# Kernel optimization log

Measured on AMD Instinct MI355X. Metric: run time of the kernel, lower is better.

## Reference

```python
import jax, jax.numpy as jnp
import numpy as np

L, H = 2, 512  # num_layers, hidden_dim (== input_dim)

def setup_inputs() -> dict:
    key = jax.random.key(0)
    ks = jax.random.split(key, 9)
    T, B, D = 1024, 64, 512
    s = 0.05  # scale randn params to keep gates non-saturated
    return {
        "x":   jax.random.normal(ks[0], (T, B, D), jnp.float32),
        "Wii": jax.random.normal(ks[1], (L, 3 * H, D), jnp.float32) * s,
        "Wic": jax.random.normal(ks[2], (L, 3 * H, H), jnp.float32) * s,
        "Wih": jax.random.normal(ks[3], (L, 3 * H, H), jnp.float32) * s,
        "bii": jax.random.normal(ks[4], (L, 3 * H), jnp.float32) * s,
        "bic": jax.random.normal(ks[5], (L, 3 * H), jnp.float32) * s,
        "bih": jax.random.normal(ks[6], (L, 3 * H), jnp.float32) * s,
        "Whh": jax.random.normal(ks[7], (L, H, H), jnp.float32) * s,
        "bhh": jax.random.normal(ks[8], (L, H), jnp.float32) * s,
    }

def _res_lstm_layer(xs, Wii, Wic, Wih, bii, bic, bih, Whh, bhh):
    # xs: [T, B, D]; input_size == hidden_size so residual is identity add.
    T, B, _ = xs.shape
    bias = bii + bic + bih  # fold the three gate biases once
    def step(carry, x_t):
        hx, cx = carry
        gates = (jnp.matmul(x_t, Wii.T) + jnp.matmul(hx, Wih.T)
                 + jnp.matmul(cx, Wic.T) + bias)          # [B, 3H]
        i_g, f_g, o_g = jnp.split(gates, 3, axis=1)
        cellgate = jnp.tanh(jnp.matmul(hx, Whh.T) + bhh)    # [B, H]
        cy = jax.nn.sigmoid(f_g) * cx + jax.nn.sigmoid(i_g) * cellgate
        hy = jax.nn.sigmoid(o_g) * (jnp.tanh(cy) + x_t)     # residual
        return (hy, cy), hy
    init = (jnp.zeros((B, H), xs.dtype), jnp.zeros((B, H), xs.dtype))
    (h, c), outs = jax.lax.scan(step, init, xs)
    return outs, h, c

def reference(x, Wii, Wic, Wih, bii, bic, bih, Whh, bhh):
    outs = x
    h_list, c_list = [], []
    for l in range(L):  # small fixed layer count
        outs, h, c = _res_lstm_layer(outs, Wii[l], Wic[l], Wih[l],
                                     bii[l], bic[l], bih[l], Whh[l], bhh[l])
        h_list.append(h)
        c_list.append(c)
    h_n = jnp.stack(h_list, axis=0)  # [L, B, H]
    c_n = jnp.stack(c_list, axis=0)
    return outs, h_n, c_n
```

## Files before the change

kernel.cpp:

```cpp
#include <hip/hip_runtime.h>
#include <cstdint>

typedef unsigned short u16;
typedef unsigned int   u32;
typedef __bf16 v8bf  __attribute__((ext_vector_type(8)));
typedef float  v4f   __attribute__((ext_vector_type(4)));
typedef u32    u32x2 __attribute__((ext_vector_type(2)));
typedef u32    u32x4 __attribute__((ext_vector_type(4)));

#define T_STEPS 1024
#define G3 1536

#define OFF_RING0 0ull
#define OFF_RING1 1048576ull
#define OFF_XBF   0ull
#define OFF_XG    67108864ull
#define OFF_WII   268435456ull
#define OFF_WPACK 270008320ull
#define OFF_WPK2  277348352ull
#define OFF_BIASF 278921216ull

__device__ __forceinline__ u16 f2b(float f) {
  u32 u = __builtin_bit_cast(u32, f);
  u += 0x7fffu + ((u >> 16) & 1u);
  return (u16)(u >> 16);
}
__device__ __forceinline__ float b2f(u16 h) {
  u32 u = ((u32)h) << 16;
  return __builtin_bit_cast(float, u);
}
__device__ __forceinline__ float sigm(float x) { return 1.0f / (1.0f + __expf(-x)); }


__global__ void k_cvt(const float* __restrict__ s, u16* __restrict__ d, int n4) {
  int i = blockIdx.x * blockDim.x + threadIdx.x;
  int st = gridDim.x * blockDim.x;
  for (; i < n4; i += st) {
    float4 v = reinterpret_cast<const float4*>(s)[i];
    u32 lo = (u32)f2b(v.x) | ((u32)f2b(v.y) << 16);
    u32 hi = (u32)f2b(v.z) | ((u32)f2b(v.w) << 16);
    uint2 pk; pk.x = lo; pk.y = hi;
    reinterpret_cast<uint2*>(d)[i] = pk;
  }
}

__global__ void k_fold(const float* __restrict__ a, const float* __restrict__ b,
                       const float* __restrict__ c, float* __restrict__ o, int n) {
  int i = blockIdx.x * blockDim.x + threadIdx.x;
  if (i < n) o[i] = a[i] + b[i] + c[i];
}

__global__ void k_pack(const float* __restrict__ Wih, const float* __restrict__ Wic,
                       const float* __restrict__ Whh, u16* __restrict__ wp) {
  int t = blockIdx.x * blockDim.x + threadIdx.x;
  if (t >= 2 * 32 * 112 * 64) return;
  int lane = t & 63; int rest = t >> 6;
  int c = rest % 112; rest /= 112;
  int s = rest & 31; int l = rest >> 5;
  int col16 = lane & 15, kq = lane >> 4;
  const float* src;
  if (c < 96) {
    int tau = c >> 5, kk = c & 31;
    int col = tau * 512 + s * 16 + col16;
    int k = kk * 32 + kq * 8;
    src = (k < 512) ? (Wih + ((size_t)l * G3 + col) * 512 + k)
                    : (Wic + ((size_t)l * G3 + col) * 512 + (k - 512));
  } else {
    int kk = c - 96;
    int col = s * 16 + col16;
    int k = kk * 32 + kq * 8;
    src = Whh + ((size_t)l * 512 + col) * 512 + k;
  }
  u16 o[8];
#pragma unroll
  for (int i = 0; i < 8; ++i) o[i] = f2b(src[i]);
  uint4 v;
  v.x = (u32)o[0] | ((u32)o[1] << 16);
  v.y = (u32)o[2] | ((u32)o[3] << 16);
  v.z = (u32)o[4] | ((u32)o[5] << 16);
  v.w = (u32)o[6] | ((u32)o[7] << 16);
  reinterpret_cast<uint4*>(wp)[t] = v;
}

__global__ void k_pack2(const float* __restrict__ Wii, u16* __restrict__ wp2) {
  int t = blockIdx.x * blockDim.x + threadIdx.x;
  if (t >= 32 * 3 * 16 * 64) return;
  int lane = t & 63;
  int kk = (t >> 6) & 15;
  int w = (t >> 10) % 3;
  int s = t / 3072;
  int col = w * 512 + s * 16 + (lane & 15);
  int k = kk * 32 + (lane >> 4) * 8;
  const float* src = Wii + ((size_t)G3 + col) * 512 + k;
  u16 o[8];
#pragma unroll
  for (int i = 0; i < 8; ++i) o[i] = f2b(src[i]);
  uint4 v;
  v.x = (u32)o[0] | ((u32)o[1] << 16);
  v.y = (u32)o[2] | ((u32)o[3] << 16);
  v.z = (u32)o[4] | ((u32)o[5] << 16);
  v.w = (u32)o[6] | ((u32)o[7] << 16);
  reinterpret_cast<uint4*>(wp2)[t] = v;
}


__global__ __launch_bounds__(256) void k_gemm(const u16* __restrict__ A,
                                              const u16* __restrict__ Bt,
                                              u16* __restrict__ C) {
  __shared__ u16 As[128 * 40];
  __shared__ u16 Bs[128 * 40];
  int m0 = blockIdx.x * 128, n0 = blockIdx.y * 128;
  int tid = threadIdx.x, lane = tid & 63, w = tid >> 6, wr = w >> 1, wc = w & 1;
  int rl = lane & 15, kq = lane >> 4;
  v4f acc[4][4] = {};
  for (int k0 = 0; k0 < 512; k0 += 32) {
#pragma unroll
    for (int c = tid; c < 1024; c += 256) {
      int row = (c & 511) >> 2, q = c & 3;
      const u16* src = (c < 512) ? (A + (size_t)(m0 + row) * 512 + k0 + q * 8)
                                 : (Bt + (size_t)(n0 + row) * 512 + k0 + q * 8);
      uint4 v = *reinterpret_cast<const uint4*>(src);
      u16* dst = (c < 512) ? (As + row * 40 + q * 8) : (Bs + row * 40 + q * 8);
      *reinterpret_cast<uint4*>(dst) = v;
    }
    __syncthreads();
    v8bf a[4], b[4];
#pragma unroll
    for (int mi = 0; mi < 4; ++mi)
      a[mi] = *reinterpret_cast<const v8bf*>(As + (wr * 64 + mi * 16 + rl) * 40 + kq * 8);
#pragma unroll
    for (int ni = 0; ni < 4; ++ni)
      b[ni] = *reinterpret_cast<const v8bf*>(Bs + (wc * 64 + ni * 16 + rl) * 40 + kq * 8);
#pragma unroll
    for (int mi = 0; mi < 4; ++mi)
#pragma unroll
      for (int ni = 0; ni < 4; ++ni)
        acc[mi][ni] = __builtin_amdgcn_mfma_f32_16x16x32_bf16(a[mi], b[ni], acc[mi][ni], 0, 0, 0);
    __syncthreads();
  }
#pragma unroll
  for (int mi = 0; mi < 4; ++mi)
#pragma unroll
    for (int ni = 0; ni < 4; ++ni)
#pragma unroll
      for (int r = 0; r < 4; ++r) {
        int row = m0 + wr * 64 + mi * 16 + kq * 4 + r;
        int col = n0 + wc * 64 + ni * 16 + rl;
        C[(size_t)row * G3 + col] = f2b(acc[mi][ni][r]);
      }
}


__global__ __launch_bounds__(512, 1) void k_lstm(
    const u16* __restrict__ xg, const u16* __restrict__ wp, const u16* __restrict__ wp2,
    const float* __restrict__ biasf, const float* __restrict__ bhh,
    const float* __restrict__ xin, float* __restrict__ outs,
    float* __restrict__ hn, float* __restrict__ cn,
    char* __restrict__ ring0, char* __restrict__ ring1) {
  extern __shared__ char lds[];
  u16* alds   = (u16*)lds;
  float* olds = (float*)(lds + 65792);
  u16* w1lds  = (u16*)(lds + 73984);
  int tid = threadIdx.x, lane = tid & 63, w = tid >> 6;
  int w2 = w >> 1, half = w & 1;
  int blk = blockIdx.x, g = blk >> 5, s = blk & 31;

  int erow = (tid >> 4) & 15, ecol = tid & 15;
  int bglob = g * 16 + erow, hcol = s * 16 + ecol;
  int col16 = lane & 15, kq = lane >> 4;
  bool isGate = (w2 < 3);
  float bias0 = 0.0f, bias1 = 0.0f;
  int cbase, nch;
  if (isGate) {
    cbase = w2 * 32 + half * 16; nch = 16;
    if (half == 0) {
      bias0 = biasf[w2 * 512 + s * 16 + col16];
      bias1 = biasf[1536 + w2 * 512 + s * 16 + col16];
    }
  } else {
    cbase = 96 + half * 8; nch = 8;
    if (half == 0) {
      bias0 = bhh[s * 16 + col16];
      bias1 = bhh[512 + s * 16 + col16];
    }
  }
  int colglob = w2 * 512 + s * 16 + col16;

  const u16* w0src = wp + (size_t)s * 57344 + (size_t)cbase * 512 + lane * 8;
  const u16* w1src = wp + 1835008 + (size_t)s * 57344 + (size_t)cbase * 512 + lane * 8;
  v8bf breg0[16], breg1[16];
  if (isGate) {
#pragma unroll
    for (int kk = 0; kk < 16; ++kk) {
      breg0[kk] = *reinterpret_cast<const v8bf*>(w0src + kk * 512);
      breg1[kk] = *reinterpret_cast<const v8bf*>(w1src + kk * 512);
    }
  } else {
#pragma unroll
    for (int kk = 0; kk < 8; ++kk) {
      breg0[kk] = *reinterpret_cast<const v8bf*>(w0src + kk * 512);
      breg1[kk] = *reinterpret_cast<const v8bf*>(w1src + kk * 512);
    }
  }
  {
    const uint4* src = reinterpret_cast<const uint4*>(wp2) + (size_t)s * 3072;
    for (int i = tid; i < 3072; i += 512)
      reinterpret_cast<uint4*>(w1lds)[i] = src[i];
  }
  float c0 = 0.0f, c1 = 0.0f;
  __syncthreads();

  auto Af = [&](int base, int kg) {
    return *reinterpret_cast<const v8bf*>(alds + col16 * 2056 + base + kg * 32 + kq * 8);
  };

  for (int t = 0; t <= T_STEPS; ++t) {
    bool doL0 = (t < T_STEPS), doL1 = (t > 0);

    float seed0[4] = {0.f, 0.f, 0.f, 0.f};
    float xi0 = 0.0f;
    if (doL0) {
      if (isGate) {
        if (half == 0) {
          const u16* xgp = xg + (size_t)(t * 64 + g * 16 + kq * 4) * G3 + colglob;
#pragma unroll
          for (int r4 = 0; r4 < 4; ++r4) seed0[r4] = b2f(xgp[(size_t)r4 * G3]) + bias0;
        }
      } else if (half == 0) {
#pragma unroll
        for (int r4 = 0; r4 < 4; ++r4) seed0[r4] = bias0;
      }
      if (tid < 256) xi0 = xin[(size_t)(t * 64 + bglob) * 512 + hcol];
    }

    u32x4 r[8];
    {
      const char* pb = ring0 + ((size_t)(t & 3) * 4 + g) * 65536 + (size_t)tid * 16;
      u32 exp = (u32)t; bool ok = false; u32 it = 0;
      while (!ok) {
#pragma unroll
        for (int i = 0; i < 8; ++i)
          asm volatile("global_load_dwordx4 %0, %1, off sc0 sc1"
                       : "=v"(r[i]) : "v"(pb + (size_t)i * 8192) : "memory");
        asm volatile("s_waitcnt vmcnt(0)" ::: "memory");
        __builtin_amdgcn_sched_barrier(0);
        ok = true;
#pragma unroll
        for (int i = 0; i < 8; ++i) ok = ok && (r[i][1] == exp) && (r[i][3] == exp);
        if (!ok) { if (++it > (1u << 11)) break; __builtin_amdgcn_s_sleep(1); }
      }
      __builtin_amdgcn_sched_barrier(0);
#pragma unroll
      for (int i = 0; i < 8; ++i) {
        int p = tid + i * 512;
        int row = p >> 8, c2 = p & 255;
        u32 hw = (r[i][0] & 0xffffu) | (r[i][2] << 16);
        u32 cw = (r[i][0] >> 16) | (r[i][2] & 0xffff0000u);
        *reinterpret_cast<u32*>(alds + row * 2056 + 2 * c2) = hw;
        *reinterpret_cast<u32*>(alds + row * 2056 + 512 + 2 * c2) = cw;
      }
    }

    u32x4 r2[8];
    if (doL1) {
      const char* pb = ring1 + ((size_t)((t - 1) & 3) * 4 + g) * 65536 + (size_t)tid * 16;
#pragma unroll
      for (int i = 0; i < 8; ++i)
        asm volatile("global_load_dwordx4 %0, %1, off sc0 sc1"
                     : "=v"(r2[i]) : "v"(pb + (size_t)i * 8192) : "memory");
    }
    __syncthreads();

    if (doL0) {
      v4f ac0, ac1, ac2, ac3;
#pragma unroll
      for (int r4 = 0; r4 < 4; ++r4) { ac0[r4] = seed0[r4]; ac1[r4] = 0.f; ac2[r4] = 0.f; ac3[r4] = 0.f; }
      if (isGate) {
#pragma unroll
        for (int kk = 0; kk < 16; kk += 4) {
          int kg = half * 16 + kk;
          ac0 = __builtin_amdgcn_mfma_f32_16x16x32_bf16(Af(0, kg + 0), breg0[kk + 0], ac0, 0, 0, 0);
          ac1 = __builtin_amdgcn_mfma_f32_16x16x32_bf16(Af(0, kg + 1), breg0[kk + 1], ac1, 0, 0, 0);
          ac2 = __builtin_amdgcn_mfma_f32_16x16x32_bf16(Af(0, kg + 2), breg0[kk + 2], ac2, 0, 0, 0);
          ac3 = __builtin_amdgcn_mfma_f32_16x16x32_bf16(Af(0, kg + 3), breg0[kk + 3], ac3, 0, 0, 0);
        }
      } else {
#pragma unroll
        for (int kk = 0; kk < 8; kk += 4) {
          int kg = half * 8 + kk;
          ac0 = __builtin_amdgcn_mfma_f32_16x16x32_bf16(Af(0, kg + 0), breg0[kk + 0], ac0, 0, 0, 0);
          ac1 = __builtin_amdgcn_mfma_f32_16x16x32_bf16(Af(0, kg + 1), breg0[kk + 1], ac1, 0, 0, 0);
          ac2 = __builtin_amdgcn_mfma_f32_16x16x32_bf16(Af(0, kg + 2), breg0[kk + 2], ac2, 0, 0, 0);
          ac3 = __builtin_amdgcn_mfma_f32_16x16x32_bf16(Af(0, kg + 3), breg0[kk + 3], ac3, 0, 0, 0);
        }
      }
      v4f acc;
#pragma unroll
      for (int r4 = 0; r4 < 4; ++r4) acc[r4] = (ac0[r4] + ac1[r4]) + (ac2[r4] + ac3[r4]);
#pragma unroll
      for (int r4 = 0; r4 < 4; ++r4) olds[w * 256 + (kq * 4 + r4) * 16 + col16] = acc[r4];
      __syncthreads();

      if (tid < 256) {
        float gi = olds[tid] + olds[256 + tid];
        float gf = olds[512 + tid] + olds[768 + tid];
        float go = olds[1024 + tid] + olds[1280 + tid];
        float gg = olds[1536 + tid] + olds[1792 + tid];
        float i_s = sigm(gi), f_s = sigm(gf), o_s = sigm(go);
        float cg = tanhf(gg);
        float cy = f_s * c0 + i_s * cg;
        float hy = o_s * (tanhf(cy) + xi0);
        c0 = cy;
        u16 hyb = f2b(hy), cyb = f2b(cy);
        u32x2 pkt;
        pkt[0] = (u32)hyb | ((u32)cyb << 16);
        pkt[1] = (u32)(t + 1);
        void* pd = ring0 + ((size_t)((t + 1) & 3) * 4 + g) * 65536
                   + (size_t)(erow * 512 + hcol) * 8;
        asm volatile("global_store_dwordx2 %0, %1, off sc0 sc1"
                     :: "v"(pd), "v"(pkt) : "memory");
        if (t == T_STEPS - 1) {
          hn[bglob * 512 + hcol] = hy;
          cn[bglob * 512 + hcol] = cy;
        }
      }
    }

    if (doL1) {
      float xi1 = (tid < 256) ? b2f(alds[erow * 2056 + hcol]) : 0.0f;

      {
        const char* pb = ring1 + ((size_t)((t - 1) & 3) * 4 + g) * 65536 + (size_t)tid * 16;
        u32 exp = (u32)(t - 1); u32 it = 0;
        for (;;) {
          asm volatile("s_waitcnt vmcnt(0)" ::: "memory");
          __builtin_amdgcn_sched_barrier(0);
          bool ok = true;
#pragma unroll
          for (int i = 0; i < 8; ++i) ok = ok && (r2[i][1] == exp) && (r2[i][3] == exp);
          if (ok) break;
          if (++it > (1u << 11)) break;
          __builtin_amdgcn_s_sleep(1);
#pragma unroll
          for (int i = 0; i < 8; ++i)
            asm volatile("global_load_dwordx4 %0, %1, off sc0 sc1"
                         : "=v"(r2[i]) : "v"(pb + (size_t)i * 8192) : "memory");
        }
        __builtin_amdgcn_sched_barrier(0);
#pragma unroll
        for (int i = 0; i < 8; ++i) {
          int p = tid + i * 512;
          int row = p >> 8, c2 = p & 255;
          u32 hw = (r2[i][0] & 0xffffu) | (r2[i][2] << 16);
          u32 cw = (r2[i][0] >> 16) | (r2[i][2] & 0xffff0000u);
          *reinterpret_cast<u32*>(alds + row * 2056 + 1024 + 2 * c2) = hw;
          *reinterpret_cast<u32*>(alds + row * 2056 + 1536 + 2 * c2) = cw;
        }
      }
      __syncthreads();

      v4f ac0, ac1, ac2, ac3;
#pragma unroll
      for (int r4 = 0; r4 < 4; ++r4) { ac0[r4] = bias1; ac1[r4] = 0.f; ac2[r4] = 0.f; ac3[r4] = 0.f; }
      if (isGate) {
#pragma unroll
        for (int kk = 0; kk < 16; kk += 4) {
          int kg = half * 16 + kk;
          ac0 = __builtin_amdgcn_mfma_f32_16x16x32_bf16(Af(1024, kg + 0), breg1[kk + 0], ac0, 0, 0, 0);
          ac1 = __builtin_amdgcn_mfma_f32_16x16x32_bf16(Af(1024, kg + 1), breg1[kk + 1], ac1, 0, 0, 0);
          ac2 = __builtin_amdgcn_mfma_f32_16x16x32_bf16(Af(1024, kg + 2), breg1[kk + 2], ac2, 0, 0, 0);
          ac3 = __builtin_amdgcn_mfma_f32_16x16x32_bf16(Af(1024, kg + 3), breg1[kk + 3], ac3, 0, 0, 0);
        }
#pragma unroll
        for (int kx = 0; kx < 8; kx += 4) {
          int kg = half * 8 + kx;
          ac0 = __builtin_amdgcn_mfma_f32_16x16x32_bf16(Af(0, kg + 0),
                  *reinterpret_cast<const v8bf*>(w1lds + ((w2 * 16 + kg + 0) * 64 + lane) * 8), ac0, 0, 0, 0);
          ac1 = __builtin_amdgcn_mfma_f32_16x16x32_bf16(Af(0, kg + 1),
                  *reinterpret_cast<const v8bf*>(w1lds + ((w2 * 16 + kg + 1) * 64 + lane) * 8), ac1, 0, 0, 0);
          ac2 = __builtin_amdgcn_mfma_f32_16x16x32_bf16(Af(0, kg + 2),
                  *reinterpret_cast<const v8bf*>(w1lds + ((w2 * 16 + kg + 2) * 64 + lane) * 8), ac2, 0, 0, 0);
          ac3 = __builtin_amdgcn_mfma_f32_16x16x32_bf16(Af(0, kg + 3),
                  *reinterpret_cast<const v8bf*>(w1lds + ((w2 * 16 + kg + 3) * 64 + lane) * 8), ac3, 0, 0, 0);
        }
      } else {
#pragma unroll
        for (int kk = 0; kk < 8; kk += 4) {
          int kg = half * 8 + kk;
          ac0 = __builtin_amdgcn_mfma_f32_16x16x32_bf16(Af(1024, kg + 0), breg1[kk + 0], ac0, 0, 0, 0);
          ac1 = __builtin_amdgcn_mfma_f32_16x16x32_bf16(Af(1024, kg + 1), breg1[kk + 1], ac1, 0, 0, 0);
          ac2 = __builtin_amdgcn_mfma_f32_16x16x32_bf16(Af(1024, kg + 2), breg1[kk + 2], ac2, 0, 0, 0);
          ac3 = __builtin_amdgcn_mfma_f32_16x16x32_bf16(Af(1024, kg + 3), breg1[kk + 3], ac3, 0, 0, 0);
        }
      }
      v4f acc;
#pragma unroll
      for (int r4 = 0; r4 < 4; ++r4) acc[r4] = (ac0[r4] + ac1[r4]) + (ac2[r4] + ac3[r4]);
#pragma unroll
      for (int r4 = 0; r4 < 4; ++r4) olds[w * 256 + (kq * 4 + r4) * 16 + col16] = acc[r4];
      __syncthreads();

      if (tid < 256) {
        float gi = olds[tid] + olds[256 + tid];
        float gf = olds[512 + tid] + olds[768 + tid];
        float go = olds[1024 + tid] + olds[1280 + tid];
        float gg = olds[1536 + tid] + olds[1792 + tid];
        float i_s = sigm(gi), f_s = sigm(gf), o_s = sigm(go);
        float cg = tanhf(gg);
        float cy = f_s * c1 + i_s * cg;
        float hy = o_s * (tanhf(cy) + xi1);
        c1 = cy;
        u16 hyb = f2b(hy), cyb = f2b(cy);
        u32x2 pkt;
        pkt[0] = (u32)hyb | ((u32)cyb << 16);
        pkt[1] = (u32)t;
        void* pd = ring1 + ((size_t)(t & 3) * 4 + g) * 65536
                   + (size_t)(erow * 512 + hcol) * 8;
        asm volatile("global_store_dwordx2 %0, %1, off sc0 sc1"
                     :: "v"(pd), "v"(pkt) : "memory");
        outs[(size_t)((t - 1) * 64 + bglob) * 512 + hcol] = hy;
        if (t == T_STEPS) {
          hn[32768 + bglob * 512 + hcol] = hy;
          cn[32768 + bglob * 512 + hcol] = cy;
        }
      }
    }
    __syncthreads();
  }
}


extern "C" void kernel_launch(void* const* d_in, const int* in_sizes, int n_in,
                              void* d_out, int out_size, void* d_ws, size_t ws_size,
                              hipStream_t stream) {
  const float* x   = (const float*)d_in[0];
  const float* Wii = (const float*)d_in[1];
  const float* Wic = (const float*)d_in[2];
  const float* Wih = (const float*)d_in[3];
  const float* bii = (const float*)d_in[4];
  const float* bic = (const float*)d_in[5];
  const float* bih = (const float*)d_in[6];
  const float* Whh = (const float*)d_in[7];
  const float* bhh = (const float*)d_in[8];
  float* out = (float*)d_out;
  char* ws = (char*)d_ws;

  u16* xbf     = (u16*)(ws + OFF_XBF);
  u16* xgb     = (u16*)(ws + OFF_XG);
  u16* wiib    = (u16*)(ws + OFF_WII);
  u16* wpack   = (u16*)(ws + OFF_WPACK);
  u16* wpk2    = (u16*)(ws + OFF_WPK2);
  float* biasf = (float*)(ws + OFF_BIASF);

  hipFuncSetAttribute(reinterpret_cast<const void*>(k_lstm),
                      hipFuncAttributeMaxDynamicSharedMemorySize, 123136);

  k_cvt <<<2048, 256, 0, stream>>>(x, xbf, 8388608);
  k_cvt <<<768, 256, 0, stream>>>(Wii, wiib, 196608);
  k_fold<<<12, 256, 0, stream>>>(bii, bic, bih, biasf, 3072);
  k_pack<<<1792, 256, 0, stream>>>(Wih, Wic, Whh, wpack);
  k_pack2<<<384, 256, 0, stream>>>(Wii, wpk2);
  k_gemm<<<dim3(512, 12), 256, 0, stream>>>(xbf, wiib, xgb);

  hipMemsetAsync(ws + OFF_RING0, 0, 2097152, stream);

  float* hn = out + 33554432;
  float* cn = out + 33554432 + 65536;
  k_lstm<<<128, 512, 123136, stream>>>(
      xgb, wpack, wpk2, biasf, bhh, x, out, hn, cn,
      ws + OFF_RING0, ws + OFF_RING1);
}
```

Measured before the change: 5.538 ms.

## Split layer-0 and layer-1 across wave groups with LDS counter sync

Waves 0-3 now handle layer 0 and waves 4-7 handle layer 1, so both layers' matvecs run concurrently instead of one after the other. Each wave holds a full K range of weights in registers, which removes the split-K partial-sum reduction. The two ring polls are merged into one loop that retries only the slices not yet ready. The per-layer __syncthreads is replaced by LDS atomic counters with spin-waits, at the cost of twice the register weights per wave and the risk of busy-wait contention.

```diff
diff --git a/kernel.cpp b/kernel.cpp
--- a/kernel.cpp
+++ b/kernel.cpp
@@ -161,53 +161,41 @@
   u16* alds   = (u16*)lds;
   float* olds = (float*)(lds + 65792);
   u16* w1lds  = (u16*)(lds + 73984);
+  u32* scnt   = (u32*)(lds + 123136);
   int tid = threadIdx.x, lane = tid & 63, w = tid >> 6;
-  int w2 = w >> 1, half = w & 1;
+  bool isL1 = w >= 4;
+  int wg = w & 3;
   int blk = blockIdx.x, g = blk >> 5, s = blk & 31;
 
-  int erow = (tid >> 4) & 15, ecol = tid & 15;
+  int et = tid & 255;
+  int erow = et >> 4, ecol = et & 15;
   int bglob = g * 16 + erow, hcol = s * 16 + ecol;
   int col16 = lane & 15, kq = lane >> 4;
-  bool isGate = (w2 < 3);
-  float bias0 = 0.0f, bias1 = 0.0f;
-  int cbase, nch;
+  bool isGate = (wg < 3);
+  float bias_w;
+  int cbase, nfr;
   if (isGate) {
-    cbase = w2 * 32 + half * 16; nch = 16;
-    if (half == 0) {
-      bias0 = biasf[w2 * 512 + s * 16 + col16];
-      bias1 = biasf[1536 + w2 * 512 + s * 16 + col16];
-    }
+    cbase = wg * 32; nfr = 32;
+    bias_w = biasf[(isL1 ? 1536 : 0) + wg * 512 + s * 16 + col16];
   } else {
-    cbase = 96 + half * 8; nch = 8;
-    if (half == 0) {
-      bias0 = bhh[s * 16 + col16];
-      bias1 = bhh[512 + s * 16 + col16];
-    }
-  }
-  int colglob = w2 * 512 + s * 16 + col16;
-
-  const u16* w0src = wp + (size_t)s * 57344 + (size_t)cbase * 512 + lane * 8;
-  const u16* w1src = wp + 1835008 + (size_t)s * 57344 + (size_t)cbase * 512 + lane * 8;
-  v8bf breg0[16], breg1[16];
-  if (isGate) {
-#pragma unroll
-    for (int kk = 0; kk < 16; ++kk) {
-      breg0[kk] = *reinterpret_cast<const v8bf*>(w0src + kk * 512);
-      breg1[kk] = *reinterpret_cast<const v8bf*>(w1src + kk * 512);
-    }
-  } else {
-#pragma unroll
-    for (int kk = 0; kk < 8; ++kk) {
-      breg0[kk] = *reinterpret_cast<const v8bf*>(w0src + kk * 512);
-      breg1[kk] = *reinterpret_cast<const v8bf*>(w1src + kk * 512);
-    }
-  }
+    cbase = 96; nfr = 16;
+    bias_w = bhh[(isL1 ? 512 : 0) + s * 16 + col16];
+  }
+  int colglob = wg * 512 + s * 16 + col16;
+
+  const u16* wsrc = wp + (isL1 ? 1835008u : 0u) + (size_t)s * 57344
+                    + (size_t)cbase * 512 + lane * 8;
+  v8bf breg[32];
+#pragma unroll
+  for (int kk = 0; kk < 32; ++kk)
+    if (kk < nfr) breg[kk] = *reinterpret_cast<const v8bf*>(wsrc + kk * 512);
   {
     const uint4* src = reinterpret_cast<const uint4*>(wp2) + (size_t)s * 3072;
     for (int i = tid; i < 3072; i += 512)
       reinterpret_cast<uint4*>(w1lds)[i] = src[i];
   }
-  float c0 = 0.0f, c1 = 0.0f;
+  if (tid < 2) scnt[tid] = 0;
+  float c_st = 0.0f;
   __syncthreads();
 
   auto Af = [&](int base, int kg) {
@@ -217,100 +205,114 @@
   for (int t = 0; t <= T_STEPS; ++t) {
     bool doL0 = (t < T_STEPS), doL1 = (t > 0);
 
-    float seed0[4] = {0.f, 0.f, 0.f, 0.f};
+    float seed[4] = {0.f, 0.f, 0.f, 0.f};
     float xi0 = 0.0f;
-    if (doL0) {
+    if (!isL1 && doL0) {
       if (isGate) {
-        if (half == 0) {
-          const u16* xgp = xg + (size_t)(t * 64 + g * 16 + kq * 4) * G3 + colglob;
-#pragma unroll
-          for (int r4 = 0; r4 < 4; ++r4) seed0[r4] = b2f(xgp[(size_t)r4 * G3]) + bias0;
-        }
-      } else if (half == 0) {
-#pragma unroll
-        for (int r4 = 0; r4 < 4; ++r4) seed0[r4] = bias0;
+        const u16* xgp = xg + (size_t)(t * 64 + g * 16 + kq * 4) * G3 + colglob;
+#pragma unroll
+        for (int r4 = 0; r4 < 4; ++r4) seed[r4] = b2f(xgp[(size_t)r4 * G3]) + bias_w;
+      } else {
+#pragma unroll
+        for (int r4 = 0; r4 < 4; ++r4) seed[r4] = bias_w;
       }
       if (tid < 256) xi0 = xin[(size_t)(t * 64 + bglob) * 512 + hcol];
     }
 
-    u32x4 r[8];
+    u32x4 r0[8], r1[8];
     {
-      const char* pb = ring0 + ((size_t)(t & 3) * 4 + g) * 65536 + (size_t)tid * 16;
-      u32 exp = (u32)t; bool ok = false; u32 it = 0;
-      while (!ok) {
-#pragma unroll
-        for (int i = 0; i < 8; ++i)
+      const char* pb0 = ring0 + ((size_t)(t & 3) * 4 + g) * 65536 + (size_t)tid * 16;
+      const char* pb1 = ring1 + ((size_t)((t - 1) & 3) * 4 + g) * 65536 + (size_t)tid * 16;
+      u32 exp0 = (u32)t, exp1 = (u32)(t - 1);
+      u32 m0 = 0xffu, m1 = doL1 ? 0xffu : 0u;
+      u32 it = 0;
+      for (;;) {
+#pragma unroll
+        for (int i = 0; i < 8; ++i) if ((m0 >> i) & 1)
           asm volatile("global_load_dwordx4 %0, %1, off sc0 sc1"
-                       : "=v"(r[i]) : "v"(pb + (size_t)i * 8192) : "memory");
+                       : "=v"(r0[i]) : "v"(pb0 + (size_t)i * 8192) : "memory");
+#pragma unroll
+        for (int i = 0; i < 8; ++i) if ((m1 >> i) & 1)
+          asm volatile("global_load_dwordx4 %0, %1, off sc0 sc1"
+                       : "=v"(r1[i]) : "v"(pb1 + (size_t)i * 8192) : "memory");
         asm volatile("s_waitcnt vmcnt(0)" ::: "memory");
         __builtin_amdgcn_sched_barrier(0);
-        ok = true;
-#pragma unroll
-        for (int i = 0; i < 8; ++i) ok = ok && (r[i][1] == exp) && (r[i][3] == exp);
-        if (!ok) { if (++it > (1u << 11)) break; __builtin_amdgcn_s_sleep(1); }
+#pragma unroll
+        for (int i = 0; i < 8; ++i)
+          if ((r0[i][1] == exp0) && (r0[i][3] == exp0)) m0 &= ~(1u << i);
+#pragma unroll
+        for (int i = 0; i < 8; ++i)
+          if ((r1[i][1] == exp1) && (r1[i][3] == exp1)) m1 &= ~(1u << i);
+        if (!(m0 | m1)) break;
+        if (++it > (1u << 11)) break;
+        __builtin_amdgcn_s_sleep(1);
       }
       __builtin_amdgcn_sched_barrier(0);
 #pragma unroll
       for (int i = 0; i < 8; ++i) {
         int p = tid + i * 512;
         int row = p >> 8, c2 = p & 255;
-        u32 hw = (r[i][0] & 0xffffu) | (r[i][2] << 16);
-        u32 cw = (r[i][0] >> 16) | (r[i][2] & 0xffff0000u);
+        u32 hw = (r0[i][0] & 0xffffu) | (r0[i][2] << 16);
+        u32 cw = (r0[i][0] >> 16) | (r0[i][2] & 0xffff0000u);
         *reinterpret_cast<u32*>(alds + row * 2056 + 2 * c2) = hw;
         *reinterpret_cast<u32*>(alds + row * 2056 + 512 + 2 * c2) = cw;
       }
-    }
-
-    u32x4 r2[8];
-    if (doL1) {
-      const char* pb = ring1 + ((size_t)((t - 1) & 3) * 4 + g) * 65536 + (size_t)tid * 16;
-#pragma unroll
-      for (int i = 0; i < 8; ++i)
-        asm volatile("global_load_dwordx4 %0, %1, off sc0 sc1"
-                     : "=v"(r2[i]) : "v"(pb + (size_t)i * 8192) : "memory");
+      if (doL1) {
+#pragma unroll
+        for (int i = 0; i < 8; ++i) {
+          int p = tid + i * 512;
+          int row = p >> 8, c2 = p & 255;
+          u32 hw = (r1[i][0] & 0xffffu) | (r1[i][2] << 16);
+          u32 cw = (r1[i][0] >> 16) | (r1[i][2] & 0xffff0000u);
+          *reinterpret_cast<u32*>(alds + row * 2056 + 1024 + 2 * c2) = hw;
+          *reinterpret_cast<u32*>(alds + row * 2056 + 1536 + 2 * c2) = cw;
+        }
+      }
     }
     __syncthreads();
 
-    if (doL0) {
-      v4f ac0, ac1, ac2, ac3;
-#pragma unroll
-      for (int r4 = 0; r4 < 4; ++r4) { ac0[r4] = seed0[r4]; ac1[r4] = 0.f; ac2[r4] = 0.f; ac3[r4] = 0.f; }
-      if (isGate) {
-#pragma unroll
-        for (int kk = 0; kk < 16; kk += 4) {
-          int kg = half * 16 + kk;
-          ac0 = __builtin_amdgcn_mfma_f32_16x16x32_bf16(Af(0, kg + 0), breg0[kk + 0], ac0, 0, 0, 0);
-          ac1 = __builtin_amdgcn_mfma_f32_16x16x32_bf16(Af(0, kg + 1), breg0[kk + 1], ac1, 0, 0, 0);
-          ac2 = __builtin_amdgcn_mfma_f32_16x16x32_bf16(Af(0, kg + 2), breg0[kk + 2], ac2, 0, 0, 0);
-          ac3 = __builtin_amdgcn_mfma_f32_16x16x32_bf16(Af(0, kg + 3), breg0[kk + 3], ac3, 0, 0, 0);
-        }
-      } else {
-#pragma unroll
-        for (int kk = 0; kk < 8; kk += 4) {
-          int kg = half * 8 + kk;
-          ac0 = __builtin_amdgcn_mfma_f32_16x16x32_bf16(Af(0, kg + 0), breg0[kk + 0], ac0, 0, 0, 0);
-          ac1 = __builtin_amdgcn_mfma_f32_16x16x32_bf16(Af(0, kg + 1), breg0[kk + 1], ac1, 0, 0, 0);
-          ac2 = __builtin_amdgcn_mfma_f32_16x16x32_bf16(Af(0, kg + 2), breg0[kk + 2], ac2, 0, 0, 0);
-          ac3 = __builtin_amdgcn_mfma_f32_16x16x32_bf16(Af(0, kg + 3), breg0[kk + 3], ac3, 0, 0, 0);
-        }
-      }
-      v4f acc;
-#pragma unroll
-      for (int r4 = 0; r4 < 4; ++r4) acc[r4] = (ac0[r4] + ac1[r4]) + (ac2[r4] + ac3[r4]);
-#pragma unroll
-      for (int r4 = 0; r4 < 4; ++r4) olds[w * 256 + (kq * 4 + r4) * 16 + col16] = acc[r4];
-      __syncthreads();
-
-      if (tid < 256) {
-        float gi = olds[tid] + olds[256 + tid];
-        float gf = olds[512 + tid] + olds[768 + tid];
-        float go = olds[1024 + tid] + olds[1280 + tid];
-        float gg = olds[1536 + tid] + olds[1792 + tid];
+    if (!isL1) {
+      if (doL0) {
+        v4f ac0, ac1, ac2, ac3;
+#pragma unroll
+        for (int r4 = 0; r4 < 4; ++r4) { ac0[r4] = seed[r4]; ac1[r4] = 0.f; ac2[r4] = 0.f; ac3[r4] = 0.f; }
+        if (isGate) {
+#pragma unroll
+          for (int kk = 0; kk < 32; kk += 4) {
+            ac0 = __builtin_amdgcn_mfma_f32_16x16x32_bf16(Af(0, kk + 0), breg[kk + 0], ac0, 0, 0, 0);
+            ac1 = __builtin_amdgcn_mfma_f32_16x16x32_bf16(Af(0, kk + 1), breg[kk + 1], ac1, 0, 0, 0);
+            ac2 = __builtin_amdgcn_mfma_f32_16x16x32_bf16(Af(0, kk + 2), breg[kk + 2], ac2, 0, 0, 0);
+            ac3 = __builtin_amdgcn_mfma_f32_16x16x32_bf16(Af(0, kk + 3), breg[kk + 3], ac3, 0, 0, 0);
+          }
+        } else {
+#pragma unroll
+          for (int kk = 0; kk < 16; kk += 4) {
+            ac0 = __builtin_amdgcn_mfma_f32_16x16x32_bf16(Af(0, kk + 0), breg[kk + 0], ac0, 0, 0, 0);
+            ac1 = __builtin_amdgcn_mfma_f32_16x16x32_bf16(Af(0, kk + 1), breg[kk + 1], ac1, 0, 0, 0);
+            ac2 = __builtin_amdgcn_mfma_f32_16x16x32_bf16(Af(0, kk + 2), breg[kk + 2], ac2, 0, 0, 0);
+            ac3 = __builtin_amdgcn_mfma_f32_16x16x32_bf16(Af(0, kk + 3), breg[kk + 3], ac3, 0, 0, 0);
+          }
+        }
+        v4f acc;
+#pragma unroll
+        for (int r4 = 0; r4 < 4; ++r4) acc[r4] = (ac0[r4] + ac1[r4]) + (ac2[r4] + ac3[r4]);
+#pragma unroll
+        for (int r4 = 0; r4 < 4; ++r4) olds[wg * 256 + (kq * 4 + r4) * 16 + col16] = acc[r4];
+        asm volatile("s_waitcnt lgkmcnt(0)" ::: "memory");
+        if (lane == 0) atomicAdd(&scnt[0], 1u);
+        {
+          volatile u32* vc = &scnt[0];
+          u32 tgt = 4u * (u32)(t + 1);
+          while (*vc < tgt) {}
+        }
+        __builtin_amdgcn_sched_barrier(0);
+
+        float gi = olds[et], gf = olds[256 + et], go = olds[512 + et], gg = olds[768 + et];
         float i_s = sigm(gi), f_s = sigm(gf), o_s = sigm(go);
         float cg = tanhf(gg);
-        float cy = f_s * c0 + i_s * cg;
+        float cy = f_s * c_st + i_s * cg;
         float hy = o_s * (tanhf(cy) + xi0);
-        c0 = cy;
+        c_st = cy;
         u16 hyb = f2b(hy), cyb = f2b(cy);
         u32x2 pkt;
         pkt[0] = (u32)hyb | ((u32)cyb << 16);
@@ -324,92 +326,60 @@
           cn[bglob * 512 + hcol] = cy;
         }
       }
-    }
-
-    if (doL1) {
-      float xi1 = (tid < 256) ? b2f(alds[erow * 2056 + hcol]) : 0.0f;
-
-      {
-        const char* pb = ring1 + ((size_t)((t - 1) & 3) * 4 + g) * 65536 + (size_t)tid * 16;
-        u32 exp = (u32)(t - 1); u32 it = 0;
-        for (;;) {
-          asm volatile("s_waitcnt vmcnt(0)" ::: "memory");
-          __builtin_amdgcn_sched_barrier(0);
-          bool ok = true;
-#pragma unroll
-          for (int i = 0; i < 8; ++i) ok = ok && (r2[i][1] == exp) && (r2[i][3] == exp);
-          if (ok) break;
-          if (++it > (1u << 11)) break;
-          __builtin_amdgcn_s_sleep(1);
-#pragma unroll
-          for (int i = 0; i < 8; ++i)
-            asm volatile("global_load_dwordx4 %0, %1, off sc0 sc1"
-                         : "=v"(r2[i]) : "v"(pb + (size_t)i * 8192) : "memory");
+    } else {
+      if (doL1) {
+        float xi1 = b2f(alds[erow * 2056 + hcol]);
+        v4f ac0, ac1, ac2, ac3;
+#pragma unroll
+        for (int r4 = 0; r4 < 4; ++r4) { ac0[r4] = bias_w; ac1[r4] = 0.f; ac2[r4] = 0.f; ac3[r4] = 0.f; }
+        if (isGate) {
+#pragma unroll
+          for (int kk = 0; kk < 32; kk += 4) {
+            ac0 = __builtin_amdgcn_mfma_f32_16x16x32_bf16(Af(1024, kk + 0), breg[kk + 0], ac0, 0, 0, 0);
+            ac1 = __builtin_amdgcn_mfma_f32_16x16x32_bf16(Af(1024, kk + 1), breg[kk + 1], ac1, 0, 0, 0);
+            ac2 = __builtin_amdgcn_mfma_f32_16x16x32_bf16(Af(1024, kk + 2), breg[kk + 2], ac2, 0, 0, 0);
+            ac3 = __builtin_amdgcn_mfma_f32_16x16x32_bf16(Af(1024, kk + 3), breg[kk + 3], ac3, 0, 0, 0);
+          }
+#pragma unroll
+          for (int kx = 0; kx < 16; kx += 4) {
+            ac0 = __builtin_amdgcn_mfma_f32_16x16x32_bf16(Af(0, kx + 0),
+                    *reinterpret_cast<const v8bf*>(w1lds + ((wg * 16 + kx + 0) * 64 + lane) * 8), ac0, 0, 0, 0);
+            ac1 = __builtin_amdgcn_mfma_f32_16x16x32_bf16(Af(0, kx + 1),
+                    *reinterpret_cast<const v8bf*>(w1lds + ((wg * 16 + kx + 1) * 64 + lane) * 8), ac1, 0, 0, 0);
+            ac2 = __builtin_amdgcn_mfma_f32_16x16x32_bf16(Af(0, kx + 2),
+                    *reinterpret_cast<const v8bf*>(w1lds + ((wg * 16 + kx + 2) * 64 + lane) * 8), ac2, 0, 0, 0);
+            ac3 = __builtin_amdgcn_mfma_f32_16x16x32_bf16(Af(0, kx + 3),
+                    *reinterpret_cast<const v8bf*>(w1lds + ((wg * 16 + kx + 3) * 64 + lane) * 8), ac3, 0, 0, 0);
+          }
+        } else {
+#pragma unroll
+          for (int kk = 0; kk < 16; kk += 4) {
+            ac0 = __builtin_amdgcn_mfma_f32_16x16x32_bf16(Af(1024, kk + 0), breg[kk + 0], ac0, 0, 0, 0);
+            ac1 = __builtin_amdgcn_mfma_f32_16x16x32_bf16(Af(1024, kk + 1), breg[kk + 1], ac1, 0, 0, 0);
+            ac2 = __builtin_amdgcn_mfma_f32_16x16x32_bf16(Af(1024, kk + 2), breg[kk + 2], ac2, 0, 0, 0);
+            ac3 = __builtin_amdgcn_mfma_f32_16x16x32_bf16(Af(1024, kk + 3), breg[kk + 3], ac3, 0, 0, 0);
+          }
+        }
+        v4f acc;
+#pragma unroll
+        for (int r4 = 0; r4 < 4; ++r4) acc[r4] = (ac0[r4] + ac1[r4]) + (ac2[r4] + ac3[r4]);
+#pragma unroll
+        for (int r4 = 0; r4 < 4; ++r4) olds[1024 + wg * 256 + (kq * 4 + r4) * 16 + col16] = acc[r4];
+        asm volatile("s_waitcnt lgkmcnt(0)" ::: "memory");
+        if (lane == 0) atomicAdd(&scnt[1], 1u);
+        {
+          volatile u32* vc = &scnt[1];
+          u32 tgt = 4u * (u32)t;
+          while (*vc < tgt) {}
         }
         __builtin_amdgcn_sched_barrier(0);
-#pragma unroll
-        for (int i = 0; i < 8; ++i) {
-          int p = tid + i * 512;
-          int row = p >> 8, c2 = p & 255;
-          u32 hw = (r2[i][0] & 0xffffu) | (r2[i][2] << 16);
-          u32 cw = (r2[i][0] >> 16) | (r2[i][2] & 0xffff0000u);
-          *reinterpret_cast<u32*>(alds + row * 2056 + 1024 + 2 * c2) = hw;
-          *reinterpret_cast<u32*>(alds + row * 2056 + 1536 + 2 * c2) = cw;
-        }
-      }
-      __syncthreads();
-
-      v4f ac0, ac1, ac2, ac3;
-#pragma unroll
-      for (int r4 = 0; r4 < 4; ++r4) { ac0[r4] = bias1; ac1[r4] = 0.f; ac2[r4] = 0.f; ac3[r4] = 0.f; }
-      if (isGate) {
-#pragma unroll
-        for (int kk = 0; kk < 16; kk += 4) {
-          int kg = half * 16 + kk;
-          ac0 = __builtin_amdgcn_mfma_f32_16x16x32_bf16(Af(1024, kg + 0), breg1[kk + 0], ac0, 0, 0, 0);
-          ac1 = __builtin_amdgcn_mfma_f32_16x16x32_bf16(Af(1024, kg + 1), breg1[kk + 1], ac1, 0, 0, 0);
-          ac2 = __builtin_amdgcn_mfma_f32_16x16x32_bf16(Af(1024, kg + 2), breg1[kk + 2], ac2, 0, 0, 0);
-          ac3 = __builtin_amdgcn_mfma_f32_16x16x32_bf16(Af(1024, kg + 3), breg1[kk + 3], ac3, 0, 0, 0);
-        }
-#pragma unroll
-        for (int kx = 0; kx < 8; kx += 4) {
-          int kg = half * 8 + kx;
-          ac0 = __builtin_amdgcn_mfma_f32_16x16x32_bf16(Af(0, kg + 0),
-                  *reinterpret_cast<const v8bf*>(w1lds + ((w2 * 16 + kg + 0) * 64 + lane) * 8), ac0, 0, 0, 0);
-          ac1 = __builtin_amdgcn_mfma_f32_16x16x32_bf16(Af(0, kg + 1),
-                  *reinterpret_cast<const v8bf*>(w1lds + ((w2 * 16 + kg + 1) * 64 + lane) * 8), ac1, 0, 0, 0);
-          ac2 = __builtin_amdgcn_mfma_f32_16x16x32_bf16(Af(0, kg + 2),
-                  *reinterpret_cast<const v8bf*>(w1lds + ((w2 * 16 + kg + 2) * 64 + lane) * 8), ac2, 0, 0, 0);
-          ac3 = __builtin_amdgcn_mfma_f32_16x16x32_bf16(Af(0, kg + 3),
-                  *reinterpret_cast<const v8bf*>(w1lds + ((w2 * 16 + kg + 3) * 64 + lane) * 8), ac3, 0, 0, 0);
-        }
-      } else {
-#pragma unroll
-        for (int kk = 0; kk < 8; kk += 4) {
-          int kg = half * 8 + kk;
-          ac0 = __builtin_amdgcn_mfma_f32_16x16x32_bf16(Af(1024, kg + 0), breg1[kk + 0], ac0, 0, 0, 0);
-          ac1 = __builtin_amdgcn_mfma_f32_16x16x32_bf16(Af(1024, kg + 1), breg1[kk + 1], ac1, 0, 0, 0);
-          ac2 = __builtin_amdgcn_mfma_f32_16x16x32_bf16(Af(1024, kg + 2), breg1[kk + 2], ac2, 0, 0, 0);
-          ac3 = __builtin_amdgcn_mfma_f32_16x16x32_bf16(Af(1024, kg + 3), breg1[kk + 3], ac3, 0, 0, 0);
-        }
-      }
-      v4f acc;
-#pragma unroll
-      for (int r4 = 0; r4 < 4; ++r4) acc[r4] = (ac0[r4] + ac1[r4]) + (ac2[r4] + ac3[r4]);
-#pragma unroll
-      for (int r4 = 0; r4 < 4; ++r4) olds[w * 256 + (kq * 4 + r4) * 16 + col16] = acc[r4];
-      __syncthreads();
-
-      if (tid < 256) {
-        float gi = olds[tid] + olds[256 + tid];
-        float gf = olds[512 + tid] + olds[768 + tid];
-        float go = olds[1024 + tid] + olds[1280 + tid];
-        float gg = olds[1536 + tid] + olds[1792 + tid];
+
+        float gi = olds[1024 + et], gf = olds[1280 + et], go = olds[1536 + et], gg = olds[1792 + et];
         float i_s = sigm(gi), f_s = sigm(gf), o_s = sigm(go);
         float cg = tanhf(gg);
-        float cy = f_s * c1 + i_s * cg;
+        float cy = f_s * c_st + i_s * cg;
         float hy = o_s * (tanhf(cy) + xi1);
-        c1 = cy;
+        c_st = cy;
         u16 hyb = f2b(hy), cyb = f2b(cy);
         u32x2 pkt;
         pkt[0] = (u32)hyb | ((u32)cyb << 16);
@@ -453,7 +423,7 @@
   float* biasf = (float*)(ws + OFF_BIASF);
 
   hipFuncSetAttribute(reinterpret_cast<const void*>(k_lstm),
-                      hipFuncAttributeMaxDynamicSharedMemorySize, 123136);
+                      hipFuncAttributeMaxDynamicSharedMemorySize, 123152);
 
   k_cvt <<<2048, 256, 0, stream>>>(x, xbf, 8388608);
   k_cvt <<<768, 256, 0, stream>>>(Wii, wiib, 196608);
@@ -466,7 +436,7 @@
 
   float* hn = out + 33554432;
   float* cn = out + 33554432 + 65536;
-  k_lstm<<<128, 512, 123136, stream>>>(
+  k_lstm<<<128, 512, 123152, stream>>>(
       xgb, wpack, wpk2, biasf, bhh, x, out, hn, cn,
       ws + OFF_RING0, ws + OFF_RING1);
 }
```

Result: slower. 5.944 ms, median of 2 (+7.3%).

## Replace per-element tagged ring packets with per-wave flag counters and merged phases

Applied to the files above, without the earlier changes.

Cross-block exchange of h/c state switches from 8-byte tagged packets, where every element carries the step number and is polled, to plain bf16 data in the ring plus a small array of per-wave flag words that consumers poll before one bulk load. This halves ring traffic and shrinks the poll to two dwords per lane. The layer-0 and layer-1 gate epilogues are also restructured so both layers' MFMA results go to separate LDS regions and share barriers, which removes some __syncthreads per step. In exchange, producers must wait for their data stores to complete before publishing the flag, adding a store-then-flag latency on the critical path.

```diff
diff --git a/kernel.cpp b/kernel.cpp
--- a/kernel.cpp
+++ b/kernel.cpp
@@ -5,20 +5,21 @@
 typedef unsigned int   u32;
 typedef __bf16 v8bf  __attribute__((ext_vector_type(8)));
 typedef float  v4f   __attribute__((ext_vector_type(4)));
-typedef u32    u32x2 __attribute__((ext_vector_type(2)));
 typedef u32    u32x4 __attribute__((ext_vector_type(4)));
 
 #define T_STEPS 1024
 #define G3 1536
 
-#define OFF_RING0 0ull
-#define OFF_RING1 1048576ull
-#define OFF_XBF   0ull
-#define OFF_XG    67108864ull
-#define OFF_WII   268435456ull
-#define OFF_WPACK 270008320ull
-#define OFF_WPK2  277348352ull
-#define OFF_BIASF 278921216ull
+#define OFF_RING0  0ull
+#define OFF_RING1  524288ull
+#define OFF_FLAGS0 1048576ull
+#define OFF_FLAGS1 1050624ull
+#define OFF_XBF    0ull
+#define OFF_XG     67108864ull
+#define OFF_WII    268435456ull
+#define OFF_WPACK  270008320ull
+#define OFF_WPK2   277348352ull
+#define OFF_BIASF  278921216ull
 
 __device__ __forceinline__ u16 f2b(float f) {
   u32 u = __builtin_bit_cast(u32, f);
@@ -156,11 +157,12 @@
     const float* __restrict__ biasf, const float* __restrict__ bhh,
     const float* __restrict__ xin, float* __restrict__ outs,
     float* __restrict__ hn, float* __restrict__ cn,
-    char* __restrict__ ring0, char* __restrict__ ring1) {
+    char* __restrict__ ring0, char* __restrict__ ring1,
+    u32* __restrict__ flags0, u32* __restrict__ flags1) {
   extern __shared__ char lds[];
   u16* alds   = (u16*)lds;
   float* olds = (float*)(lds + 65792);
-  u16* w1lds  = (u16*)(lds + 73984);
+  u16* w1lds  = (u16*)(lds + 82176);
   int tid = threadIdx.x, lane = tid & 63, w = tid >> 6;
   int w2 = w >> 1, half = w & 1;
   int blk = blockIdx.x, g = blk >> 5, s = blk & 31;
@@ -170,15 +172,15 @@
   int col16 = lane & 15, kq = lane >> 4;
   bool isGate = (w2 < 3);
   float bias0 = 0.0f, bias1 = 0.0f;
-  int cbase, nch;
+  int cbase;
   if (isGate) {
-    cbase = w2 * 32 + half * 16; nch = 16;
+    cbase = w2 * 32 + half * 16;
     if (half == 0) {
       bias0 = biasf[w2 * 512 + s * 16 + col16];
       bias1 = biasf[1536 + w2 * 512 + s * 16 + col16];
     }
   } else {
-    cbase = 96 + half * 8; nch = 8;
+    cbase = 96 + half * 8;
     if (half == 0) {
       bias0 = bhh[s * 16 + col16];
       bias1 = bhh[512 + s * 16 + col16];
@@ -210,6 +212,10 @@
   float c0 = 0.0f, c1 = 0.0f;
   __syncthreads();
 
+  const u32* fb0 = flags0 + g * 128;
+  const u32* fb1 = flags1 + g * 128;
+  int prow = tid >> 5, pcb = (tid & 31) * 32;
+
   auto Af = [&](int base, int kg) {
     return *reinterpret_cast<const v8bf*>(alds + col16 * 2056 + base + kg * 32 + kq * 8);
   };
@@ -220,54 +226,46 @@
     float seed0[4] = {0.f, 0.f, 0.f, 0.f};
     float xi0 = 0.0f;
     if (doL0) {
-      if (isGate) {
-        if (half == 0) {
+      if (half == 0) {
+        if (isGate) {
           const u16* xgp = xg + (size_t)(t * 64 + g * 16 + kq * 4) * G3 + colglob;
 #pragma unroll
           for (int r4 = 0; r4 < 4; ++r4) seed0[r4] = b2f(xgp[(size_t)r4 * G3]) + bias0;
-        }
-      } else if (half == 0) {
-#pragma unroll
-        for (int r4 = 0; r4 < 4; ++r4) seed0[r4] = bias0;
+        } else {
+#pragma unroll
+          for (int r4 = 0; r4 < 4; ++r4) seed0[r4] = bias0;
+        }
       }
       if (tid < 256) xi0 = xin[(size_t)(t * 64 + bglob) * 512 + hcol];
     }
 
-    u32x4 r[8];
     {
-      const char* pb = ring0 + ((size_t)(t & 3) * 4 + g) * 65536 + (size_t)tid * 16;
-      u32 exp = (u32)t; bool ok = false; u32 it = 0;
-      while (!ok) {
-#pragma unroll
-        for (int i = 0; i < 8; ++i)
-          asm volatile("global_load_dwordx4 %0, %1, off sc0 sc1"
-                       : "=v"(r[i]) : "v"(pb + (size_t)i * 8192) : "memory");
+      u32 tgt = (u32)t; u32 it = 0;
+      for (;;) {
+        u32 f0, f1;
+        asm volatile("global_load_dword %0, %1, off sc0 sc1"
+                     : "=v"(f0) : "v"(fb0 + lane) : "memory");
+        asm volatile("global_load_dword %0, %1, off sc0 sc1"
+                     : "=v"(f1) : "v"(fb0 + 64 + lane) : "memory");
         asm volatile("s_waitcnt vmcnt(0)" ::: "memory");
-        __builtin_amdgcn_sched_barrier(0);
-        ok = true;
-#pragma unroll
-        for (int i = 0; i < 8; ++i) ok = ok && (r[i][1] == exp) && (r[i][3] == exp);
-        if (!ok) { if (++it > (1u << 11)) break; __builtin_amdgcn_s_sleep(1); }
+        if (__all((f0 >= tgt) && (f1 >= tgt))) break;
+        if (++it > (1u << 12)) break;
+        __builtin_amdgcn_s_sleep(1);
       }
       __builtin_amdgcn_sched_barrier(0);
-#pragma unroll
-      for (int i = 0; i < 8; ++i) {
-        int p = tid + i * 512;
-        int row = p >> 8, c2 = p & 255;
-        u32 hw = (r[i][0] & 0xffffu) | (r[i][2] << 16);
-        u32 cw = (r[i][0] >> 16) | (r[i][2] & 0xffff0000u);
-        *reinterpret_cast<u32*>(alds + row * 2056 + 2 * c2) = hw;
-        *reinterpret_cast<u32*>(alds + row * 2056 + 512 + 2 * c2) = cw;
-      }
-    }
-
-    u32x4 r2[8];
-    if (doL1) {
-      const char* pb = ring1 + ((size_t)((t - 1) & 3) * 4 + g) * 65536 + (size_t)tid * 16;
-#pragma unroll
-      for (int i = 0; i < 8; ++i)
+    }
+    {
+      const char* pb = ring0 + ((size_t)(t & 3) * 4 + g) * 32768 + (size_t)tid * 64;
+      u32x4 p[4];
+#pragma unroll
+      for (int k = 0; k < 4; ++k)
         asm volatile("global_load_dwordx4 %0, %1, off sc0 sc1"
-                     : "=v"(r2[i]) : "v"(pb + (size_t)i * 8192) : "memory");
+                     : "=v"(p[k]) : "v"(pb + k * 16) : "memory");
+      asm volatile("s_waitcnt vmcnt(0)" ::: "memory");
+      __builtin_amdgcn_sched_barrier(0);
+#pragma unroll
+      for (int k = 0; k < 4; ++k)
+        *reinterpret_cast<u32x4*>(alds + prow * 2056 + pcb + k * 8) = p[k];
     }
     __syncthreads();
 
@@ -299,66 +297,65 @@
       for (int r4 = 0; r4 < 4; ++r4) acc[r4] = (ac0[r4] + ac1[r4]) + (ac2[r4] + ac3[r4]);
 #pragma unroll
       for (int r4 = 0; r4 < 4; ++r4) olds[w * 256 + (kq * 4 + r4) * 16 + col16] = acc[r4];
-      __syncthreads();
-
-      if (tid < 256) {
-        float gi = olds[tid] + olds[256 + tid];
-        float gf = olds[512 + tid] + olds[768 + tid];
-        float go = olds[1024 + tid] + olds[1280 + tid];
-        float gg = olds[1536 + tid] + olds[1792 + tid];
-        float i_s = sigm(gi), f_s = sigm(gf), o_s = sigm(go);
-        float cg = tanhf(gg);
-        float cy = f_s * c0 + i_s * cg;
-        float hy = o_s * (tanhf(cy) + xi0);
-        c0 = cy;
-        u16 hyb = f2b(hy), cyb = f2b(cy);
-        u32x2 pkt;
-        pkt[0] = (u32)hyb | ((u32)cyb << 16);
-        pkt[1] = (u32)(t + 1);
-        void* pd = ring0 + ((size_t)((t + 1) & 3) * 4 + g) * 65536
-                   + (size_t)(erow * 512 + hcol) * 8;
-        asm volatile("global_store_dwordx2 %0, %1, off sc0 sc1"
-                     :: "v"(pd), "v"(pkt) : "memory");
-        if (t == T_STEPS - 1) {
-          hn[bglob * 512 + hcol] = hy;
-          cn[bglob * 512 + hcol] = cy;
-        }
-      }
     }
 
     if (doL1) {
-      float xi1 = (tid < 256) ? b2f(alds[erow * 2056 + hcol]) : 0.0f;
-
-      {
-        const char* pb = ring1 + ((size_t)((t - 1) & 3) * 4 + g) * 65536 + (size_t)tid * 16;
-        u32 exp = (u32)(t - 1); u32 it = 0;
-        for (;;) {
-          asm volatile("s_waitcnt vmcnt(0)" ::: "memory");
-          __builtin_amdgcn_sched_barrier(0);
-          bool ok = true;
-#pragma unroll
-          for (int i = 0; i < 8; ++i) ok = ok && (r2[i][1] == exp) && (r2[i][3] == exp);
-          if (ok) break;
-          if (++it > (1u << 11)) break;
-          __builtin_amdgcn_s_sleep(1);
-#pragma unroll
-          for (int i = 0; i < 8; ++i)
-            asm volatile("global_load_dwordx4 %0, %1, off sc0 sc1"
-                         : "=v"(r2[i]) : "v"(pb + (size_t)i * 8192) : "memory");
-        }
-        __builtin_amdgcn_sched_barrier(0);
-#pragma unroll
-        for (int i = 0; i < 8; ++i) {
-          int p = tid + i * 512;
-          int row = p >> 8, c2 = p & 255;
-          u32 hw = (r2[i][0] & 0xffffu) | (r2[i][2] << 16);
-          u32 cw = (r2[i][0] >> 16) | (r2[i][2] & 0xffff0000u);
-          *reinterpret_cast<u32*>(alds + row * 2056 + 1024 + 2 * c2) = hw;
-          *reinterpret_cast<u32*>(alds + row * 2056 + 1536 + 2 * c2) = cw;
-        }
-      }
-      __syncthreads();
-
+      u32 tgt = (u32)(t - 1); u32 it = 0;
+      for (;;) {
+        u32 f0, f1;
+        asm volatile("global_load_dword %0, %1, off sc0 sc1"
+                     : "=v"(f0) : "v"(fb1 + lane) : "memory");
+        asm volatile("global_load_dword %0, %1, off sc0 sc1"
+                     : "=v"(f1) : "v"(fb1 + 64 + lane) : "memory");
+        asm volatile("s_waitcnt vmcnt(0)" ::: "memory");
+        if (__all((f0 >= tgt) && (f1 >= tgt))) break;
+        if (++it > (1u << 12)) break;
+        __builtin_amdgcn_s_sleep(1);
+      }
+      __builtin_amdgcn_sched_barrier(0);
+      const char* pb = ring1 + ((size_t)((t - 1) & 3) * 4 + g) * 32768 + (size_t)tid * 64;
+      u32x4 p[4];
+#pragma unroll
+      for (int k = 0; k < 4; ++k)
+        asm volatile("global_load_dwordx4 %0, %1, off sc0 sc1"
+                     : "=v"(p[k]) : "v"(pb + k * 16) : "memory");
+      asm volatile("s_waitcnt vmcnt(0)" ::: "memory");
+      __builtin_amdgcn_sched_barrier(0);
+#pragma unroll
+      for (int k = 0; k < 4; ++k)
+        *reinterpret_cast<u32x4*>(alds + prow * 2056 + 1024 + pcb + k * 8) = p[k];
+    }
+    __syncthreads();
+
+    if (doL0 && tid < 256) {
+      float gi = olds[tid] + olds[256 + tid];
+      float gf = olds[512 + tid] + olds[768 + tid];
+      float go = olds[1024 + tid] + olds[1280 + tid];
+      float gg = olds[1536 + tid] + olds[1792 + tid];
+      float i_s = sigm(gi), f_s = sigm(gf), o_s = sigm(go);
+      float cg = tanhf(gg);
+      float cy = f_s * c0 + i_s * cg;
+      float hy = o_s * (tanhf(cy) + xi0);
+      c0 = cy;
+      u16 hyb = f2b(hy), cyb = f2b(cy);
+      char* rb = ring0 + ((size_t)((t + 1) & 3) * 4 + g) * 32768;
+      void* ph = rb + (size_t)(erow * 1024 + hcol) * 2;
+      void* pc = rb + (size_t)(erow * 1024 + 512 + hcol) * 2;
+      asm volatile("global_store_short %0, %1, off sc0 sc1" :: "v"(ph), "v"((u32)hyb) : "memory");
+      asm volatile("global_store_short %0, %1, off sc0 sc1" :: "v"(pc), "v"((u32)cyb) : "memory");
+      asm volatile("s_waitcnt vmcnt(0)" ::: "memory");
+      if (lane == 0) {
+        u32* fp = flags0 + g * 128 + s * 4 + w;
+        u32 fv = (u32)(t + 1);
+        asm volatile("global_store_dword %0, %1, off sc0 sc1" :: "v"(fp), "v"(fv) : "memory");
+      }
+      if (t == T_STEPS - 1) {
+        hn[bglob * 512 + hcol] = hy;
+        cn[bglob * 512 + hcol] = cy;
+      }
+    }
+
+    if (doL1) {
       v4f ac0, ac1, ac2, ac3;
 #pragma unroll
       for (int r4 = 0; r4 < 4; ++r4) { ac0[r4] = bias1; ac1[r4] = 0.f; ac2[r4] = 0.f; ac3[r4] = 0.f; }
@@ -397,32 +394,37 @@
 #pragma unroll
       for (int r4 = 0; r4 < 4; ++r4) acc[r4] = (ac0[r4] + ac1[r4]) + (ac2[r4] + ac3[r4]);
 #pragma unroll
-      for (int r4 = 0; r4 < 4; ++r4) olds[w * 256 + (kq * 4 + r4) * 16 + col16] = acc[r4];
-      __syncthreads();
-
-      if (tid < 256) {
-        float gi = olds[tid] + olds[256 + tid];
-        float gf = olds[512 + tid] + olds[768 + tid];
-        float go = olds[1024 + tid] + olds[1280 + tid];
-        float gg = olds[1536 + tid] + olds[1792 + tid];
-        float i_s = sigm(gi), f_s = sigm(gf), o_s = sigm(go);
-        float cg = tanhf(gg);
-        float cy = f_s * c1 + i_s * cg;
-        float hy = o_s * (tanhf(cy) + xi1);
-        c1 = cy;
-        u16 hyb = f2b(hy), cyb = f2b(cy);
-        u32x2 pkt;
-        pkt[0] = (u32)hyb | ((u32)cyb << 16);
-        pkt[1] = (u32)t;
-        void* pd = ring1 + ((size_t)(t & 3) * 4 + g) * 65536
-                   + (size_t)(erow * 512 + hcol) * 8;
-        asm volatile("global_store_dwordx2 %0, %1, off sc0 sc1"
-                     :: "v"(pd), "v"(pkt) : "memory");
-        outs[(size_t)((t - 1) * 64 + bglob) * 512 + hcol] = hy;
-        if (t == T_STEPS) {
-          hn[32768 + bglob * 512 + hcol] = hy;
-          cn[32768 + bglob * 512 + hcol] = cy;
-        }
+      for (int r4 = 0; r4 < 4; ++r4) olds[2048 + w * 256 + (kq * 4 + r4) * 16 + col16] = acc[r4];
+    }
+    __syncthreads();
+
+    if (doL1 && tid < 256) {
+      float xi1 = b2f(alds[erow * 2056 + hcol]);
+      float gi = olds[2048 + tid] + olds[2304 + tid];
+      float gf = olds[2560 + tid] + olds[2816 + tid];
+      float go = olds[3072 + tid] + olds[3328 + tid];
+      float gg = olds[3584 + tid] + olds[3840 + tid];
+      float i_s = sigm(gi), f_s = sigm(gf), o_s = sigm(go);
+      float cg = tanhf(gg);
+      float cy = f_s * c1 + i_s * cg;
+      float hy = o_s * (tanhf(cy) + xi1);
+      c1 = cy;
+      u16 hyb = f2b(hy), cyb = f2b(cy);
+      char* rb = ring1 + ((size_t)(t & 3) * 4 + g) * 32768;
+      void* ph = rb + (size_t)(erow * 1024 + hcol) * 2;
+      void* pc = rb + (size_t)(erow * 1024 + 512 + hcol) * 2;
+      asm volatile("global_store_short %0, %1, off sc0 sc1" :: "v"(ph), "v"((u32)hyb) : "memory");
+      asm volatile("global_store_short %0, %1, off sc0 sc1" :: "v"(pc), "v"((u32)cyb) : "memory");
+      asm volatile("s_waitcnt vmcnt(0)" ::: "memory");
+      if (lane == 0) {
+        u32* fp = flags1 + g * 128 + s * 4 + w;
+        u32 fv = (u32)t;
+        asm volatile("global_store_dword %0, %1, off sc0 sc1" :: "v"(fp), "v"(fv) : "memory");
+      }
+      outs[(size_t)((t - 1) * 64 + bglob) * 512 + hcol] = hy;
+      if (t == T_STEPS) {
+        hn[32768 + bglob * 512 + hcol] = hy;
+        cn[32768 + bglob * 512 + hcol] = cy;
       }
     }
     __syncthreads();
@@ -453,7 +455,7 @@
   float* biasf = (float*)(ws + OFF_BIASF);
 
   hipFuncSetAttribute(reinterpret_cast<const void*>(k_lstm),
-                      hipFuncAttributeMaxDynamicSharedMemorySize, 123136);
+                      hipFuncAttributeMaxDynamicSharedMemorySize, 131328);
 
   k_cvt <<<2048, 256, 0, stream>>>(x, xbf, 8388608);
   k_cvt <<<768, 256, 0, stream>>>(Wii, wiib, 196608);
@@ -462,11 +464,12 @@
   k_pack2<<<384, 256, 0, stream>>>(Wii, wpk2);
   k_gemm<<<dim3(512, 12), 256, 0, stream>>>(xbf, wiib, xgb);
 
-  hipMemsetAsync(ws + OFF_RING0, 0, 2097152, stream);
+  hipMemsetAsync(ws + OFF_RING0, 0, 1052672, stream);
 
   float* hn = out + 33554432;
   float* cn = out + 33554432 + 65536;
-  k_lstm<<<128, 512, 123136, stream>>>(
+  k_lstm<<<128, 512, 131328, stream>>>(
       xgb, wpack, wpk2, biasf, bhh, x, out, hn, cn,
-      ws + OFF_RING0, ws + OFF_RING1);
-}
+      ws + OFF_RING0, ws + OFF_RING1,
+      (u32*)(ws + OFF_FLAGS0), (u32*)(ws + OFF_FLAGS1));
+}
```

Measured after the change: 6.213 ms. 1.12x slower.
